# Kernel optimization log

Hardware: AMD Instinct MI355X
Metric: run time of the kernel (lower is better)

The kernel has to match this reference:

```python
import jax, jax.numpy as jnp
import numpy as np

B, T, DP, DQ, DO = 128, 2048, 256, 256, 256


def setup_inputs() -> dict:
    key = jax.random.key(0)
    ks = jax.random.split(key, 10)
    return {
        "input_p": jax.random.normal(ks[0], (B, DP), dtype=jnp.float32),
        "mask_p": jnp.ones((B,), dtype=jnp.float32),
        "input_q": jax.random.normal(ks[1], (B, T, DQ), dtype=jnp.float32),
        "mask_q": jax.random.randint(ks[2], (B, T), 0, 2, dtype=jnp.int32),
        "h_tm1": jax.random.normal(ks[3], (B, DO), dtype=jnp.float32),
        # layer-0 parameters (depth == 0)
        "W_p_r": jax.random.normal(ks[4], (DO, DP + DO), dtype=jnp.float32) * 0.04,
        "b_p_r": jnp.zeros((DO,), dtype=jnp.float32),
        "W_q": jax.random.normal(ks[5], (DO, DQ), dtype=jnp.float32) * 0.05,
        "b_q": jnp.zeros((DO,), dtype=jnp.float32),
        "w": jax.random.normal(ks[6], (DO,), dtype=jnp.float32) * 0.05,
        "match_b": jnp.ones((1,), dtype=jnp.float32),
        "depth": 0,
    }


def masked_softmax(x, m, axis=-1):
    x = jnp.clip(x, -15.0, 15.0)
    x = x * m
    e_x = jnp.exp(x - jnp.max(x, axis=axis, keepdims=True))
    e_x = e_x * m
    return e_x / (jnp.sum(e_x, axis=axis, keepdims=True) + 1e-6)


def reference(input_p, mask_p, input_q, mask_q, h_tm1, W_p_r, b_p_r, W_q, b_q, w, match_b, depth):
    mq = mask_q.astype(jnp.float32)
    # G_p_r: [B, 1, DO]
    G_p_r = (jnp.concatenate([input_p, h_tm1], axis=-1) @ W_p_r.T + b_p_r)[:, None, :]
    # G_q: [B, T, DO]
    G_q = input_q @ W_q.T + b_q
    G = jnp.tanh(G_p_r + G_q)
    alpha = jnp.einsum("btd,d->bt", G, w) + match_b  # [B, T]
    alpha = masked_softmax(alpha, mq, axis=-1)
    z = jnp.einsum("bt,btd->bd", alpha, input_q)  # bmm context
    return jnp.concatenate([input_p, z], axis=1)  # [B, DP+DQ]
```

## Files before the change

kernel.cpp:

```cpp
#include <hip/hip_runtime.h>

typedef short short8 __attribute__((ext_vector_type(8)));
typedef float floatx4 __attribute__((ext_vector_type(4)));
typedef unsigned short ushort_t;

constexpr int Bn = 128, Tn = 2048, DPn = 256, DQn = 256, DOn = 256;

__device__ inline unsigned short f2bf(float x) {
    unsigned u = __float_as_uint(x);
    u += 0x7fffu + ((u >> 16) & 1u);
    return (unsigned short)(u >> 16);
}

__device__ inline float fast_tanh(float x) {
    float e = __expf(2.0f * x);
    return 1.0f - 2.0f / (e + 1.0f);
}

__global__ __launch_bounds__(256) void cvt_wq_kernel(const float* __restrict__ wq,
                                                     unsigned short* __restrict__ wqbf) {
    int idx = blockIdx.x * 256 + threadIdx.x;
    float4 v = ((const float4*)wq)[idx];
    unsigned p0 = (unsigned)f2bf(v.x) | ((unsigned)f2bf(v.y) << 16);
    unsigned p1 = (unsigned)f2bf(v.z) | ((unsigned)f2bf(v.w) << 16);
    ((uint2*)wqbf)[idx] = make_uint2(p0, p1);
}

__global__ __launch_bounds__(256) void base_kernel(const float* __restrict__ input_p,
                                                   const float* __restrict__ h_tm1,
                                                   const float* __restrict__ Wpr,
                                                   const float* __restrict__ bpr,
                                                   const float* __restrict__ bq,
                                                   float* __restrict__ base) {
    __shared__ float v[512];
    int b = blockIdx.x, tid = threadIdx.x;
    v[tid]       = input_p[b * DPn + tid];
    v[256 + tid] = h_tm1[b * DOn + tid];
    __syncthreads();
    const float4* row = (const float4*)(Wpr + (size_t)tid * 512);
    const float4* vv  = (const float4*)v;
    float acc = 0.f;
#pragma unroll 8
    for (int i = 0; i < 128; i++) {
        float4 r = row[i], x = vv[i];
        acc = fmaf(r.x, x.x, acc);
        acc = fmaf(r.y, x.y, acc);
        acc = fmaf(r.z, x.z, acc);
        acc = fmaf(r.w, x.w, acc);
    }
    base[b * DOn + tid] = acc + bpr[tid] + bq[tid];
}

__global__ __launch_bounds__(256) void logits_kernel(const float* __restrict__ q,
                                                     const unsigned short* __restrict__ wqbf,
                                                     const float* __restrict__ base,
                                                     const float* __restrict__ wvec,
                                                     const float* __restrict__ matchb,
                                                     float* __restrict__ alpha) {
    __shared__ unsigned short qtile[64 * 264];
    __shared__ float basel[256];
    __shared__ float wl[256];
    __shared__ float partl[4][64];

    int b = blockIdx.y;
    int t0 = blockIdx.x * 64;
    int tid = threadIdx.x;

    {
        int r = tid >> 2;
        int kb = (tid & 3) * 64;
        const float* src = q + ((size_t)b * Tn + t0 + r) * DQn + kb;
        unsigned short* dst = qtile + r * 264 + kb;
#pragma unroll
        for (int i = 0; i < 16; i++) {
            float4 v = *(const float4*)(src + i * 4);
            unsigned p0 = (unsigned)f2bf(v.x) | ((unsigned)f2bf(v.y) << 16);
            unsigned p1 = (unsigned)f2bf(v.z) | ((unsigned)f2bf(v.w) << 16);
            *(uint2*)(dst + i * 4) = make_uint2(p0, p1);
        }
    }
    basel[tid] = base[b * DOn + tid];
    wl[tid] = wvec[tid];
    __syncthreads();

    int w = tid >> 6, lane = tid & 63, quad = lane >> 4, l15 = lane & 15;
    float p[4][4] = {{0.f}};
    int n0w = w * 64;

#pragma unroll
    for (int nt = 0; nt < 4; nt++) {
        int nn = n0w + nt * 16 + l15;
        short8 bfrag[8];
        const unsigned short* bp = wqbf + (size_t)nn * DQn + quad * 8;
#pragma unroll
        for (int ks = 0; ks < 8; ks++) bfrag[ks] = *(const short8*)(bp + ks * 32);
        float bn = basel[nn], wn = wl[nn];
#pragma unroll
        for (int mt = 0; mt < 4; mt++) {
            const unsigned short* ap = qtile + (mt * 16 + l15) * 264 + quad * 8;
            floatx4 acc = {0.f, 0.f, 0.f, 0.f};
#pragma unroll
            for (int ks = 0; ks < 8; ks++) {
                short8 af = *(const short8*)(ap + ks * 32);
                acc = __builtin_amdgcn_mfma_f32_16x16x32_bf16(af, bfrag[ks], acc, 0, 0, 0);
            }
#pragma unroll
            for (int r = 0; r < 4; r++) {
                float g = fast_tanh(acc[r] + bn);
                p[mt][r] = fmaf(g, wn, p[mt][r]);
            }
        }
    }
#pragma unroll
    for (int off = 1; off < 16; off <<= 1) {
#pragma unroll
        for (int mt = 0; mt < 4; mt++)
#pragma unroll
            for (int r = 0; r < 4; r++) p[mt][r] += __shfl_xor(p[mt][r], off);
    }
    if (l15 == 0) {
#pragma unroll
        for (int mt = 0; mt < 4; mt++)
#pragma unroll
            for (int r = 0; r < 4; r++) partl[w][mt * 16 + quad * 4 + r] = p[mt][r];
    }
    __syncthreads();
    if (tid < 64) {
        float lg = partl[0][tid] + partl[1][tid] + partl[2][tid] + partl[3][tid] + matchb[0];
        alpha[(size_t)b * Tn + t0 + tid] = lg;
    }
}

__global__ __launch_bounds__(256) void softmax_kernel(float* __restrict__ alpha,
                                                      const int* __restrict__ maskq) {
    __shared__ float redmax[4];
    __shared__ float redsum[4];
    int b = blockIdx.x, tid = threadIdx.x;
    int lane = tid & 63, w = tid >> 6;
    float x[8], mv[8];
    float lmax = -1e30f;
#pragma unroll
    for (int i = 0; i < 8; i++) {
        int t = tid + i * 256;
        float a = alpha[(size_t)b * Tn + t];
        float mi = (float)maskq[(size_t)b * Tn + t];
        float xi = fminf(fmaxf(a, -15.f), 15.f) * mi;
        x[i] = xi;
        mv[i] = mi;
        lmax = fmaxf(lmax, xi);
    }
#pragma unroll
    for (int off = 32; off >= 1; off >>= 1) lmax = fmaxf(lmax, __shfl_xor(lmax, off));
    if (lane == 0) redmax[w] = lmax;
    __syncthreads();
    float mx = fmaxf(fmaxf(redmax[0], redmax[1]), fmaxf(redmax[2], redmax[3]));

    float e[8];
    float lsum = 0.f;
#pragma unroll
    for (int i = 0; i < 8; i++) {
        e[i] = __expf(x[i] - mx) * mv[i];
        lsum += e[i];
    }
#pragma unroll
    for (int off = 32; off >= 1; off >>= 1) lsum += __shfl_xor(lsum, off);
    if (lane == 0) redsum[w] = lsum;
    __syncthreads();
    float s = redsum[0] + redsum[1] + redsum[2] + redsum[3];
    float inv = 1.0f / (s + 1e-6f);
#pragma unroll
    for (int i = 0; i < 8; i++) alpha[(size_t)b * Tn + tid + i * 256] = e[i] * inv;
}

__global__ __launch_bounds__(256) void zpart_kernel(const float* __restrict__ q,
                                                    const float* __restrict__ alpha,
                                                    float* __restrict__ zpart) {
    int b = blockIdx.y, c = blockIdx.x, tid = threadIdx.x;
    int t0 = c * 128;
    const float* qp = q + ((size_t)b * Tn + t0) * DQn + tid;
    const float* ap = alpha + (size_t)b * Tn + t0;
    float acc = 0.f;
#pragma unroll 4
    for (int t = 0; t < 128; t++) acc = fmaf(ap[t], qp[(size_t)t * DQn], acc);
    zpart[((size_t)b * 16 + c) * DQn + tid] = acc;
}

__global__ __launch_bounds__(256) void finalize_kernel(const float* __restrict__ input_p,
                                                       const float* __restrict__ zpart,
                                                       float* __restrict__ out) {
    int b = blockIdx.x, tid = threadIdx.x;
    out[(size_t)b * 512 + tid] = input_p[(size_t)b * DPn + tid];
    float z = 0.f;
#pragma unroll
    for (int c = 0; c < 16; c++) z += zpart[((size_t)b * 16 + c) * DQn + tid];
    out[(size_t)b * 512 + 256 + tid] = z;
}

extern "C" void kernel_launch(void* const* d_in, const int* in_sizes, int n_in,
                              void* d_out, int out_size, void* d_ws, size_t ws_size,
                              hipStream_t stream) {
    const float* input_p = (const float*)d_in[0];
    const float* input_q = (const float*)d_in[2];
    const int*   mask_q  = (const int*)d_in[3];
    const float* h_tm1   = (const float*)d_in[4];
    const float* W_p_r   = (const float*)d_in[5];
    const float* b_p_r   = (const float*)d_in[6];
    const float* W_q     = (const float*)d_in[7];
    const float* b_q     = (const float*)d_in[8];
    const float* w       = (const float*)d_in[9];
    const float* match_b = (const float*)d_in[10];
    float* out = (float*)d_out;

    char* ws = (char*)d_ws;
    unsigned short* wqbf = (unsigned short*)ws;
    float* base  = (float*)(ws + 131072);
    float* alpha = (float*)(ws + 262144);
    float* zpart = (float*)(ws + 262144 + 1048576);

    cvt_wq_kernel<<<64, 256, 0, stream>>>(W_q, wqbf);
    base_kernel<<<Bn, 256, 0, stream>>>(input_p, h_tm1, W_p_r, b_p_r, b_q, base);
    logits_kernel<<<dim3(Tn / 64, Bn), 256, 0, stream>>>(input_q, wqbf, base, w, match_b, alpha);
    softmax_kernel<<<Bn, 256, 0, stream>>>(alpha, mask_q);
    zpart_kernel<<<dim3(16, Bn), 256, 0, stream>>>(input_q, alpha, zpart);
    finalize_kernel<<<Bn, 256, 0, stream>>>(input_p, zpart, out);
}
```

Measured before the change: 508.6 us.

## Fuse logits, softmax and context reduction into one pass over input_q

Merges the logits, softmax and weighted-sum kernels into a single kernel that reads each 64-row chunk of input_q once. The bf16 tile kept in shared memory is reused for the context sum. Because the logits are clipped to at most 15, each chunk can use a fixed softmax shift of 15, so it writes partial sums and maxima and a final kernel rescales. This removes the second full read of the 256 MB input_q and the alpha round trip. In exchange the context now uses bf16-rounded q instead of fp32, and zpart partials grow to 32 per batch row.

```diff
diff --git a/kernel.cpp b/kernel.cpp
--- a/kernel.cpp
+++ b/kernel.cpp
@@ -2,16 +2,18 @@
 
 typedef short short8 __attribute__((ext_vector_type(8)));
 typedef float floatx4 __attribute__((ext_vector_type(4)));
-typedef unsigned short ushort_t;
 
 constexpr int Bn = 128, Tn = 2048, DPn = 256, DQn = 256, DOn = 256;
+constexpr int NCH = Tn / 64;
 
 __device__ inline unsigned short f2bf(float x) {
     unsigned u = __float_as_uint(x);
     u += 0x7fffu + ((u >> 16) & 1u);
     return (unsigned short)(u >> 16);
 }
-
+__device__ inline float bf2f(unsigned short h) {
+    return __uint_as_float(((unsigned)h) << 16);
+}
 __device__ inline float fast_tanh(float x) {
     float e = __expf(2.0f * x);
     return 1.0f - 2.0f / (e + 1.0f);
@@ -51,149 +53,152 @@
     base[b * DOn + tid] = acc + bpr[tid] + bq[tid];
 }
 
-__global__ __launch_bounds__(256) void logits_kernel(const float* __restrict__ q,
-                                                     const unsigned short* __restrict__ wqbf,
-                                                     const float* __restrict__ base,
-                                                     const float* __restrict__ wvec,
-                                                     const float* __restrict__ matchb,
-                                                     float* __restrict__ alpha) {
-    __shared__ unsigned short qtile[64 * 264];
-    __shared__ float basel[256];
-    __shared__ float wl[256];
+__global__ __launch_bounds__(256, 2) void fused_kernel(const float* __restrict__ q,
+                                                       const unsigned short* __restrict__ wqbf,
+                                                       const float* __restrict__ base,
+                                                       const float* __restrict__ wvec,
+                                                       const float* __restrict__ matchb,
+                                                       const int* __restrict__ maskq,
+                                                       float* __restrict__ zpart,
+                                                       float* __restrict__ spart,
+                                                       float* __restrict__ mpart) {
+    __shared__ unsigned short qtile[32 * 64 * 8];
     __shared__ float partl[4][64];
-
-    int b = blockIdx.y;
-    int t0 = blockIdx.x * 64;
+    __shared__ float earr[64];
+    __shared__ float zp[4][256];
+
+    int b = blockIdx.y, c = blockIdx.x;
+    int t0 = c * 64;
     int tid = threadIdx.x;
+    int w = tid >> 6, lane = tid & 63, l15 = lane & 15, quad = lane >> 4;
+
+    short8 bfr[4][8];
+    const unsigned short* bbase = wqbf + (size_t)(w * 64 + l15) * 256 + quad * 8;
+#pragma unroll
+    for (int nt = 0; nt < 4; nt++)
+#pragma unroll
+        for (int ks = 0; ks < 8; ks++)
+            bfr[nt][ks] = *(const short8*)(bbase + nt * 16 * 256 + ks * 32);
+    float bn[4], wn[4];
+#pragma unroll
+    for (int nt = 0; nt < 4; nt++) {
+        int n = w * 64 + nt * 16 + l15;
+        bn[nt] = base[b * DOn + n];
+        wn[nt] = wvec[n];
+    }
 
     {
-        int r = tid >> 2;
-        int kb = (tid & 3) * 64;
-        const float* src = q + ((size_t)b * Tn + t0 + r) * DQn + kb;
-        unsigned short* dst = qtile + r * 264 + kb;
-#pragma unroll
-        for (int i = 0; i < 16; i++) {
-            float4 v = *(const float4*)(src + i * 4);
-            unsigned p0 = (unsigned)f2bf(v.x) | ((unsigned)f2bf(v.y) << 16);
-            unsigned p1 = (unsigned)f2bf(v.z) | ((unsigned)f2bf(v.w) << 16);
-            *(uint2*)(dst + i * 4) = make_uint2(p0, p1);
-        }
-    }
-    basel[tid] = base[b * DOn + tid];
-    wl[tid] = wvec[tid];
-    __syncthreads();
-
-    int w = tid >> 6, lane = tid & 63, quad = lane >> 4, l15 = lane & 15;
-    float p[4][4] = {{0.f}};
-    int n0w = w * 64;
-
-#pragma unroll
-    for (int nt = 0; nt < 4; nt++) {
-        int nn = n0w + nt * 16 + l15;
-        short8 bfrag[8];
-        const unsigned short* bp = wqbf + (size_t)nn * DQn + quad * 8;
-#pragma unroll
-        for (int ks = 0; ks < 8; ks++) bfrag[ks] = *(const short8*)(bp + ks * 32);
-        float bn = basel[nn], wn = wl[nn];
-#pragma unroll
-        for (int mt = 0; mt < 4; mt++) {
-            const unsigned short* ap = qtile + (mt * 16 + l15) * 264 + quad * 8;
+        const float* src = q + ((size_t)b * Tn + t0 + w * 16 + l15) * DQn + quad * 8;
+        unsigned short* dst = qtile + ((size_t)(w * 8) * 64 + lane) * 8;
+#pragma unroll
+        for (int ks = 0; ks < 8; ks++) {
+            float4 v0 = *(const float4*)(src + ks * 32);
+            float4 v1 = *(const float4*)(src + ks * 32 + 4);
+            short8 s;
+            s[0] = (short)f2bf(v0.x); s[1] = (short)f2bf(v0.y);
+            s[2] = (short)f2bf(v0.z); s[3] = (short)f2bf(v0.w);
+            s[4] = (short)f2bf(v1.x); s[5] = (short)f2bf(v1.y);
+            s[6] = (short)f2bf(v1.z); s[7] = (short)f2bf(v1.w);
+            *(short8*)(dst + ks * 512) = s;
+        }
+    }
+    __syncthreads();
+
+#pragma unroll
+    for (int mt = 0; mt < 4; mt++) {
+        short8 af[8];
+        const unsigned short* ab = qtile + ((size_t)(mt * 8) * 64 + lane) * 8;
+#pragma unroll
+        for (int ks = 0; ks < 8; ks++) af[ks] = *(const short8*)(ab + ks * 512);
+        float prow[4] = {0.f, 0.f, 0.f, 0.f};
+#pragma unroll
+        for (int nt = 0; nt < 4; nt++) {
             floatx4 acc = {0.f, 0.f, 0.f, 0.f};
 #pragma unroll
-            for (int ks = 0; ks < 8; ks++) {
-                short8 af = *(const short8*)(ap + ks * 32);
-                acc = __builtin_amdgcn_mfma_f32_16x16x32_bf16(af, bfrag[ks], acc, 0, 0, 0);
+            for (int ks = 0; ks < 8; ks++)
+                acc = __builtin_amdgcn_mfma_f32_16x16x32_bf16(af[ks], bfr[nt][ks], acc, 0, 0, 0);
+#pragma unroll
+            for (int r = 0; r < 4; r++) {
+                float g = fast_tanh(acc[r] + bn[nt]);
+                prow[r] = fmaf(g, wn[nt], prow[r]);
             }
-#pragma unroll
-            for (int r = 0; r < 4; r++) {
-                float g = fast_tanh(acc[r] + bn);
-                p[mt][r] = fmaf(g, wn, p[mt][r]);
-            }
-        }
-    }
-#pragma unroll
-    for (int off = 1; off < 16; off <<= 1) {
-#pragma unroll
-        for (int mt = 0; mt < 4; mt++)
-#pragma unroll
-            for (int r = 0; r < 4; r++) p[mt][r] += __shfl_xor(p[mt][r], off);
-    }
-    if (l15 == 0) {
-#pragma unroll
-        for (int mt = 0; mt < 4; mt++)
-#pragma unroll
-            for (int r = 0; r < 4; r++) partl[w][mt * 16 + quad * 4 + r] = p[mt][r];
-    }
-    __syncthreads();
+        }
+#pragma unroll
+        for (int off = 1; off < 16; off <<= 1)
+#pragma unroll
+            for (int r = 0; r < 4; r++) prow[r] += __shfl_xor(prow[r], off);
+        if (l15 == 0) {
+#pragma unroll
+            for (int r = 0; r < 4; r++) partl[w][mt * 16 + quad * 4 + r] = prow[r];
+        }
+    }
+    __syncthreads();
+
     if (tid < 64) {
-        float lg = partl[0][tid] + partl[1][tid] + partl[2][tid] + partl[3][tid] + matchb[0];
-        alpha[(size_t)b * Tn + t0 + tid] = lg;
-    }
-}
-
-__global__ __launch_bounds__(256) void softmax_kernel(float* __restrict__ alpha,
-                                                      const int* __restrict__ maskq) {
-    __shared__ float redmax[4];
-    __shared__ float redsum[4];
+        int t = tid;
+        float lg = partl[0][t] + partl[1][t] + partl[2][t] + partl[3][t] + matchb[0];
+        float m = (float)maskq[(size_t)b * Tn + t0 + t];
+        float x = fminf(fmaxf(lg, -15.f), 15.f) * m;
+        float e = __expf(x - 15.f) * m;
+        earr[t] = e;
+        float xm = x, es = e;
+#pragma unroll
+        for (int off = 1; off < 64; off <<= 1) {
+            xm = fmaxf(xm, __shfl_xor(xm, off));
+            es += __shfl_xor(es, off);
+        }
+        if (t == 0) {
+            mpart[b * NCH + c] = xm;
+            spart[b * NCH + c] = es;
+        }
+    }
+    __syncthreads();
+
+    float et = earr[w * 16 + l15];
+#pragma unroll
+    for (int i = 0; i < 8; i++) {
+        short8 f = *(const short8*)(qtile + ((size_t)(w * 8 + i) * 64 + lane) * 8);
+        float v[8];
+#pragma unroll
+        for (int j = 0; j < 8; j++) v[j] = bf2f((unsigned short)f[j]) * et;
+#pragma unroll
+        for (int off = 1; off < 16; off <<= 1)
+#pragma unroll
+            for (int j = 0; j < 8; j++) v[j] += __shfl_xor(v[j], off);
+        if (l15 == 0) {
+            float* zd = &zp[w][i * 32 + quad * 8];
+            *(float4*)(zd)     = make_float4(v[0], v[1], v[2], v[3]);
+            *(float4*)(zd + 4) = make_float4(v[4], v[5], v[6], v[7]);
+        }
+    }
+    __syncthreads();
+
+    {
+        int d = tid;
+        float zs = zp[0][d] + zp[1][d] + zp[2][d] + zp[3][d];
+        zpart[((size_t)b * NCH + c) * DQn + d] = zs;
+    }
+}
+
+__global__ __launch_bounds__(256) void final_kernel(const float* __restrict__ input_p,
+                                                    const float* __restrict__ zpart,
+                                                    const float* __restrict__ spart,
+                                                    const float* __restrict__ mpart,
+                                                    float* __restrict__ out) {
     int b = blockIdx.x, tid = threadIdx.x;
-    int lane = tid & 63, w = tid >> 6;
-    float x[8], mv[8];
-    float lmax = -1e30f;
-#pragma unroll
-    for (int i = 0; i < 8; i++) {
-        int t = tid + i * 256;
-        float a = alpha[(size_t)b * Tn + t];
-        float mi = (float)maskq[(size_t)b * Tn + t];
-        float xi = fminf(fmaxf(a, -15.f), 15.f) * mi;
-        x[i] = xi;
-        mv[i] = mi;
-        lmax = fmaxf(lmax, xi);
-    }
-#pragma unroll
-    for (int off = 32; off >= 1; off >>= 1) lmax = fmaxf(lmax, __shfl_xor(lmax, off));
-    if (lane == 0) redmax[w] = lmax;
-    __syncthreads();
-    float mx = fmaxf(fmaxf(redmax[0], redmax[1]), fmaxf(redmax[2], redmax[3]));
-
-    float e[8];
-    float lsum = 0.f;
-#pragma unroll
-    for (int i = 0; i < 8; i++) {
-        e[i] = __expf(x[i] - mx) * mv[i];
-        lsum += e[i];
-    }
-#pragma unroll
-    for (int off = 32; off >= 1; off >>= 1) lsum += __shfl_xor(lsum, off);
-    if (lane == 0) redsum[w] = lsum;
-    __syncthreads();
-    float s = redsum[0] + redsum[1] + redsum[2] + redsum[3];
-    float inv = 1.0f / (s + 1e-6f);
-#pragma unroll
-    for (int i = 0; i < 8; i++) alpha[(size_t)b * Tn + tid + i * 256] = e[i] * inv;
-}
-
-__global__ __launch_bounds__(256) void zpart_kernel(const float* __restrict__ q,
-                                                    const float* __restrict__ alpha,
-                                                    float* __restrict__ zpart) {
-    int b = blockIdx.y, c = blockIdx.x, tid = threadIdx.x;
-    int t0 = c * 128;
-    const float* qp = q + ((size_t)b * Tn + t0) * DQn + tid;
-    const float* ap = alpha + (size_t)b * Tn + t0;
-    float acc = 0.f;
-#pragma unroll 4
-    for (int t = 0; t < 128; t++) acc = fmaf(ap[t], qp[(size_t)t * DQn], acc);
-    zpart[((size_t)b * 16 + c) * DQn + tid] = acc;
-}
-
-__global__ __launch_bounds__(256) void finalize_kernel(const float* __restrict__ input_p,
-                                                       const float* __restrict__ zpart,
-                                                       float* __restrict__ out) {
-    int b = blockIdx.x, tid = threadIdx.x;
+    float S = 0.f, mx = -1e30f;
+#pragma unroll 8
+    for (int c = 0; c < NCH; c++) {
+        S += spart[b * NCH + c];
+        mx = fmaxf(mx, mpart[b * NCH + c]);
+    }
+    float denom = S + 1e-6f * __expf(mx - 15.f);
+    float inv = 1.0f / denom;
+    float zs = 0.f;
+#pragma unroll 8
+    for (int c = 0; c < NCH; c++) zs += zpart[((size_t)b * NCH + c) * DQn + tid];
     out[(size_t)b * 512 + tid] = input_p[(size_t)b * DPn + tid];
-    float z = 0.f;
-#pragma unroll
-    for (int c = 0; c < 16; c++) z += zpart[((size_t)b * 16 + c) * DQn + tid];
-    out[(size_t)b * 512 + 256 + tid] = z;
+    out[(size_t)b * 512 + 256 + tid] = zs * inv;
 }
 
 extern "C" void kernel_launch(void* const* d_in, const int* in_sizes, int n_in,
@@ -214,13 +219,13 @@
     char* ws = (char*)d_ws;
     unsigned short* wqbf = (unsigned short*)ws;
     float* base  = (float*)(ws + 131072);
-    float* alpha = (float*)(ws + 262144);
-    float* zpart = (float*)(ws + 262144 + 1048576);
+    float* zpart = (float*)(ws + 262144);
+    float* spart = (float*)(ws + 262144 + 4194304);
+    float* mpart = (float*)(ws + 262144 + 4194304 + 16384);
 
     cvt_wq_kernel<<<64, 256, 0, stream>>>(W_q, wqbf);
     base_kernel<<<Bn, 256, 0, stream>>>(input_p, h_tm1, W_p_r, b_p_r, b_q, base);
-    logits_kernel<<<dim3(Tn / 64, Bn), 256, 0, stream>>>(input_q, wqbf, base, w, match_b, alpha);
-    softmax_kernel<<<Bn, 256, 0, stream>>>(alpha, mask_q);
-    zpart_kernel<<<dim3(16, Bn), 256, 0, stream>>>(input_q, alpha, zpart);
-    finalize_kernel<<<Bn, 256, 0, stream>>>(input_p, zpart, out);
-}
+    fused_kernel<<<dim3(NCH, Bn), 256, 0, stream>>>(input_q, wqbf, base, w, match_b,
+                                                    mask_q, zpart, spart, mpart);
+    final_kernel<<<Bn, 256, 0, stream>>>(input_p, zpart, spart, mpart, out);
+}
```

Result: faster. 452.0 us (-11.1%).
